# Optimization experiments

Hardware: AMD Instinct MI355X
Metric: run time of the kernel (lower is better)

## Reference

```python
import jax, jax.numpy as jnp
import numpy as np

# ---- config (YOLOv4-style, TRAIN_SIZE=608, P2..P5) ----
STRIDES = (4.0, 8.0, 16.0, 32.0)
ANCHORS = np.array([
    [[12, 16], [19, 36], [40, 28], [36, 75]],
    [[36, 75], [76, 55], [72, 146], [142, 110]],
    [[72, 146], [142, 110], [192, 243], [459, 401]],
    [[142, 110], [192, 243], [300, 300], [459, 401]],
], dtype=np.float32)  # [LEVELS, NUM_ANCHORS, 2]
MAX_PROP = 100
SCORE_THRESH = 0.25
IOU_THRESH = 0.5


def decode_prediction(p, anchors, stride):
    # p: [b, A, h, w, 6] -> [b, A*h*w, 5] with xyxy + score
    b, A, h, w, _ = p.shape
    txy, twh, conf, cls = p[..., :2], p[..., 2:4], p[..., 4:5], p[..., 5:6]
    gx, gy = jnp.meshgrid(jnp.arange(w, dtype=p.dtype), jnp.arange(h, dtype=p.dtype))
    grid = jnp.stack([gx, gy], axis=-1)[None, None]  # [1,1,h,w,2]
    xy = (jax.nn.sigmoid(txy) + grid) * stride
    wh = jnp.exp(twh) * anchors[None, :, None, None, :]
    score = jax.nn.sigmoid(conf) * jax.nn.sigmoid(cls)
    x1y1 = xy - 0.5 * wh
    x2y2 = xy + 0.5 * wh
    out = jnp.concatenate([x1y1, x2y2, score], axis=-1)  # [b,A,h,w,5]
    return out.reshape(b, A * h * w, 5)


def _iou_one_vs_all(box, boxes):
    # box: [4], boxes: [N,4] (xyxy)
    lt = jnp.maximum(box[:2], boxes[:, :2])
    rb = jnp.minimum(box[2:], boxes[:, 2:])
    wh = jnp.maximum(rb - lt, 0.0)
    inter = wh[:, 0] * wh[:, 1]
    a1 = jnp.maximum(box[2] - box[0], 0.0) * jnp.maximum(box[3] - box[1], 0.0)
    a2 = jnp.maximum(boxes[:, 2] - boxes[:, 0], 0.0) * jnp.maximum(boxes[:, 3] - boxes[:, 1], 0.0)
    return inter / (a1 + a2 - inter + 1e-9)


def _nms_single(boxes, scores):
    # greedy NMS, padded to MAX_PROP with zero rows
    s0 = jnp.where(scores >= SCORE_THRESH, scores, 0.0)

    def step(s, _):
        i = jnp.argmax(s)
        sc = s[i]
        box = boxes[i]
        keep = sc > 0.0
        row = jnp.where(keep, jnp.concatenate([box, sc[None]]), jnp.zeros(5, boxes.dtype))
        iou = _iou_one_vs_all(box, boxes)
        s = jnp.where((iou > IOU_THRESH) & keep, 0.0, s)
        s = s.at[i].set(0.0)
        return s, row

    _, props = jax.lax.scan(step, s0, None, length=MAX_PROP)
    return props  # [MAX_PROP, 5]


def entry_stop_gradients(t, mask):
    # gradient flows only through entries where mask==1
    return jax.lax.stop_gradient(t) * (1.0 - mask) + t * mask


def _forward(p2, p3, p4, p5):
    anchors = jnp.asarray(ANCHORS)
    d2 = decode_prediction(p2, anchors[0], STRIDES[0])
    d3 = decode_prediction(p3, anchors[1], STRIDES[1])
    d4 = decode_prediction(p4, anchors[2], STRIDES[2])
    d5 = decode_prediction(p5, anchors[3], STRIDES[3])
    proposals = jnp.concatenate([d2, d3, d4, d5], axis=1)  # [b, N, 5]
    proposals = jax.vmap(lambda pr: _nms_single(pr[:, :4], pr[:, 4]))(proposals)  # [b, MAX_PROP, 5]
    mask = (jnp.sum(proposals[..., :4], axis=-1) != 0.0).astype(proposals.dtype)[..., None]
    return entry_stop_gradients(proposals, mask)


def setup_inputs() -> dict:
    key = jax.random.key(0)
    k2, k3, k4, k5 = jax.random.split(key, 4)
    b, A, ch = 32, 4, 6
    return {
        "p2": jax.random.normal(k2, (b, A, 152, 152, ch), dtype=jnp.float32),
        "p3": jax.random.normal(k3, (b, A, 76, 76, ch), dtype=jnp.float32),
        "p4": jax.random.normal(k4, (b, A, 38, 38, ch), dtype=jnp.float32),
        "p5": jax.random.normal(k5, (b, A, 19, 19, ch), dtype=jnp.float32),
    }


def reference(p2, p3, p4, p5):
    return _forward(p2, p3, p4, p5)
```

## Files before the change

### kernel.cpp

```cpp
#include <hip/hip_runtime.h>
#include <cstdint>
#include <cstddef>

typedef unsigned int u32;
typedef unsigned long long u64;

#define NTOT 122740
#define NQ   30685
#define NPAIR 61370
#define KTOP 1024
#define WIN  256
#define NBIN 4096
#define SCORE_T 0.25f
#define TBITS 0x3E800000u
#define CSTRIDE 64


#define WS_COUNTERS 524288
#define WS_COMPACT  532480
#define WS_SCORES   794624

__device__ __forceinline__ float sigm(float x) { return 1.0f / (1.0f + expf(-x)); }

__device__ __forceinline__ int score_bin(u32 bits) {
  return min(4095, 1 + (int)((bits - TBITS) >> 12));
}

__device__ float4 decode_box_from_gidx(u32 gidx, int b,
    const float* __restrict__ p2, const float* __restrict__ p3,
    const float* __restrict__ p4, const float* __restrict__ p5)
{
  const float* p; int t, H, W; float stride;
  float aw0, ah0, aw1, ah1, aw2, ah2, aw3, ah3;
  if (gidx < 92416u) {
    p = p2 + (size_t)b * 92416 * 6; t = (int)gidx; H = 152; W = 152; stride = 4.0f;
    aw0=12.f; ah0=16.f; aw1=19.f; ah1=36.f; aw2=40.f; ah2=28.f; aw3=36.f; ah3=75.f;
  } else if (gidx < 115520u) {
    p = p3 + (size_t)b * 23104 * 6; t = (int)(gidx - 92416u); H = 76; W = 76; stride = 8.0f;
    aw0=36.f; ah0=75.f; aw1=76.f; ah1=55.f; aw2=72.f; ah2=146.f; aw3=142.f; ah3=110.f;
  } else if (gidx < 121296u) {
    p = p4 + (size_t)b * 5776 * 6; t = (int)(gidx - 115520u); H = 38; W = 38; stride = 16.0f;
    aw0=72.f; ah0=146.f; aw1=142.f; ah1=110.f; aw2=192.f; ah2=243.f; aw3=459.f; ah3=401.f;
  } else {
    p = p5 + (size_t)b * 1444 * 6; t = (int)(gidx - 121296u); H = 19; W = 19; stride = 32.0f;
    aw0=142.f; ah0=110.f; aw1=192.f; ah1=243.f; aw2=300.f; ah2=300.f; aw3=459.f; ah3=401.f;
  }
  int HW = H * W;
  int a = t / HW;
  int r = t - a * HW;
  int y = r / W;
  int x = r - y * W;
  const float* q = p + (size_t)t * 6;
  float2 t01 = *(const float2*)(q + 0);
  float2 t23 = *(const float2*)(q + 2);
  float cx = (sigm(t01.x) + (float)x) * stride;
  float cy = (sigm(t01.y) + (float)y) * stride;
  float aw = (a == 0) ? aw0 : (a == 1) ? aw1 : (a == 2) ? aw2 : aw3;
  float ah = (a == 0) ? ah0 : (a == 1) ? ah1 : (a == 2) ? ah2 : ah3;
  float bw = expf(t23.x) * aw;
  float bh = expf(t23.y) * ah;
  return make_float4(cx - 0.5f * bw, cy - 0.5f * bh, cx + 0.5f * bw, cy + 0.5f * bh);
}

__device__ __forceinline__ bool iou_gt(float4 A, float4 B) {
  float ltx = fmaxf(A.x, B.x), lty = fmaxf(A.y, B.y);
  float rbx = fminf(A.z, B.z), rby = fminf(A.w, B.w);
  float w = fmaxf(rbx - ltx, 0.0f), h = fmaxf(rby - lty, 0.0f);
  float inter = w * h;
  float a1 = fmaxf(A.z - A.x, 0.0f) * fmaxf(A.w - A.y, 0.0f);
  float a2 = fmaxf(B.z - B.x, 0.0f) * fmaxf(B.w - B.y, 0.0f);
  float iou = inter / (a1 + a2 - inter + 1e-9f);
  return iou > 0.5f;
}

__global__ __launch_bounds__(1024)
void zero_kernel(u32* w) {
  int t = blockIdx.x * 1024 + threadIdx.x;
  if (t < 133120) w[t] = 0u;
}

__global__ __launch_bounds__(256)
void decode_score_hist(const float* __restrict__ p2, const float* __restrict__ p3,
                       const float* __restrict__ p4, const float* __restrict__ p5,
                       u32* __restrict__ scores, u32* __restrict__ hist)
{
  __shared__ u32 lhist[NBIN];
  const int tid = threadIdx.x;
  const int b = blockIdx.y;
  for (int i = tid; i < NBIN; i += 256) lhist[i] = 0u;
  __syncthreads();

  uint2* srow = (uint2*)(scores + (size_t)b * NTOT);
  const int pbase = blockIdx.x * 2048;
  #pragma unroll 2
  for (int k = 0; k < 8; ++k) {
    int P = pbase + k * 256 + tid;
    if (P < NPAIR) {
      int t0 = 2 * P;
      const float* p; int l0, LN;
      if (t0 < 92416)       { p = p2; l0 = t0;          LN = 92416; }
      else if (t0 < 115520) { p = p3; l0 = t0 - 92416;  LN = 23104; }
      else if (t0 < 121296) { p = p4; l0 = t0 - 115520; LN = 5776;  }
      else                  { p = p5; l0 = t0 - 121296; LN = 1444;  }
      const float* q = p + ((size_t)b * LN + (size_t)l0) * 6 + 4;
      float4 v1 = *(const float4*)(q);
      float4 v2 = *(const float4*)(q + 4);
      float s0 = sigm(v1.x) * sigm(v1.y);
      float s1 = sigm(v2.z) * sigm(v2.w);
      u32 b0 = (s0 >= SCORE_T) ? __float_as_uint(s0) : 0u;
      u32 b1 = (s1 >= SCORE_T) ? __float_as_uint(s1) : 0u;
      srow[P] = make_uint2(b0, b1);
      if (b0) atomicAdd(&lhist[score_bin(b0)], 1u);
      if (b1) atomicAdd(&lhist[score_bin(b1)], 1u);
    }
  }
  __syncthreads();
  u32* gh = hist + (size_t)b * NBIN;
  for (int i = tid; i < NBIN; i += 256) {
    u32 v = lhist[i];
    if (v) atomicAdd(&gh[i], v);
  }
}

__global__ __launch_bounds__(256)
void filter_kernel(const u32* __restrict__ scores, const u32* __restrict__ hist,
                   u32* __restrict__ counters, uint2* __restrict__ compact)
{
  __shared__ u32 shist[NBIN];
  __shared__ u32 scan[256];
  __shared__ uint2 cand[KTOP];
  __shared__ u32 s_cnt, s_base;
  __shared__ int s_B;
  const int tid = threadIdx.x;
  const int b = blockIdx.y;

  const u32* gh = hist + (size_t)b * NBIN;
  for (int i = tid; i < NBIN; i += 256) shist[i] = gh[i];
  if (tid == 0) s_cnt = 0u;
  __syncthreads();

  u32 g = 0;
  const int base = tid * 16;
  #pragma unroll
  for (int k = 0; k < 16; ++k) g += shist[base + k];
  scan[tid] = g;
  __syncthreads();
  for (int off = 1; off < 256; off <<= 1) {
    u32 v = (tid + off < 256) ? scan[tid + off] : 0u;
    __syncthreads();
    scan[tid] += v;
    __syncthreads();
  }
  if (tid == 0 && scan[0] <= (u32)KTOP) s_B = 1;
  {
    u32 nxt = (tid < 255) ? scan[tid + 1] : 0u;
    if (scan[tid] > (u32)KTOP && nxt <= (u32)KTOP) {
      u32 c = nxt;
      int Bv = base + 16;
      for (int bin = base + 15; bin >= base; --bin) {
        c += shist[bin];
        if (c <= (u32)KTOP) Bv = bin; else break;
      }
      s_B = Bv;
    }
  }
  __syncthreads();
  const int B = max(s_B, 1);

  const uint4* sp = (const uint4*)(scores + (size_t)b * NTOT);
  const int i0 = blockIdx.x * 2048;
  const int i1 = min(i0 + 2048, NQ);
  for (int i = i0 + tid; i < i1; i += 256) {
    uint4 v = sp[i];
    u32 c4[4] = { v.x, v.y, v.z, v.w };
    #pragma unroll
    for (int c = 0; c < 4; ++c) {
      u32 bits = c4[c];
      if (bits && score_bin(bits) >= B) {
        u32 pos = atomicAdd(&s_cnt, 1u);
        if (pos < (u32)KTOP) cand[pos] = make_uint2(bits, (u32)(4 * i + c));
      }
    }
  }
  __syncthreads();
  const u32 m = min(s_cnt, (u32)KTOP);
  if (tid == 0) s_base = m ? atomicAdd(&counters[(size_t)b * CSTRIDE], m) : 0u;
  __syncthreads();
  const u32 gbase = s_base;
  uint2* crow = compact + (size_t)b * KTOP;
  for (u32 i = tid; i < m; i += 256) {
    u32 dst = gbase + i;
    if (dst < (u32)KTOP) crow[dst] = cand[i];
  }
}

__global__ __launch_bounds__(1024, 1)
void sort_nms_kernel(const uint2* __restrict__ compact, const u32* __restrict__ counters,
                     const float* __restrict__ p2, const float* __restrict__ p3,
                     const float* __restrict__ p4, const float* __restrict__ p5,
                     float* __restrict__ out)
{
  const int b = blockIdx.x;
  const int tid = threadIdx.x;

  __shared__ u64 skey[KTOP];
  __shared__ float4 sbox[WIN];
  __shared__ u64 smat[WIN * 4];
  __shared__ float4 selbox[100];
  __shared__ int s_misc[4];

  const int n = min((int)counters[(size_t)b * CSTRIDE], KTOP);
  const uint2* crow = compact + (size_t)b * KTOP;
  if (tid < n) {
    uint2 pr = crow[tid];
    skey[tid] = ~(((u64)pr.x << 32) | (u32)(~pr.y));
  } else {
    skey[tid] = ~0ull;
  }
  __syncthreads();

  for (int kk = 2; kk <= KTOP; kk <<= 1) {
    for (int jj = kk >> 1; jj > 0; jj >>= 1) {
      int i = tid, ixj = i ^ jj;
      if (ixj > i) {
        u64 a = skey[i], c = skey[ixj];
        bool up = ((i & kk) == 0);
        if ((a > c) == up) { skey[i] = c; skey[ixj] = a; }
      }
      __syncthreads();
    }
  }

  const int Wn = min(n, WIN);

  if (tid < WIN) {
    sbox[tid] = (tid < Wn) ? decode_box_from_gidx(~(u32)(~skey[tid]), b, p2, p3, p4, p5)
                           : make_float4(0.f, 0.f, 0.f, 0.f);
  }
  __syncthreads();

  {
    int row = tid >> 2, word = tid & 3;
    u64 bits = 0;
    if (row < Wn) {
      float4 A = sbox[row];
      int j0 = word * 64;
      int je = min(64, Wn - j0);
      for (int j = 0; j < je; ++j)
        if (iou_gt(A, sbox[j0 + j])) bits |= (1ull << j);
    }
    smat[tid] = bits;
  }
  __syncthreads();

  if (tid == 0) {
    u64 s0 = 0, s1 = 0, s2 = 0, s3 = 0;
    int sel = 0;
    for (int p = 0; p < Wn && sel < 100; ++p) {
      u64 sw = (p < 64) ? s0 : (p < 128) ? s1 : (p < 192) ? s2 : s3;
      if ((sw >> (p & 63)) & 1ull) continue;
      float4 box = sbox[p];
      u64 kcomp = ~skey[p];
      float sc = __uint_as_float((u32)(kcomp >> 32));
      selbox[sel] = box;
      float* orow = out + (size_t)b * 500 + (size_t)sel * 5;
      orow[0] = box.x; orow[1] = box.y; orow[2] = box.z; orow[3] = box.w; orow[4] = sc;
      sel++;
      s0 |= smat[p * 4 + 0]; s1 |= smat[p * 4 + 1];
      s2 |= smat[p * 4 + 2]; s3 |= smat[p * 4 + 3];
    }
    s_misc[2] = sel;
    s_misc[3] = (sel < 100 && n > WIN) ? 1 : 0;
  }
  __syncthreads();

  if (s_misc[3]) {
    if (tid < 64) {
      const int lane = tid;
      int sel = s_misc[2];
      for (int p = WIN; p < n && sel < 100; ++p) {
        u64 kcomp = ~skey[p];
        float4 box = decode_box_from_gidx(~(u32)kcomp, b, p2, p3, p4, p5);
        bool hit = false;
        if (lane < sel) hit = iou_gt(selbox[lane], box);
        if (lane + 64 < sel) hit = hit || iou_gt(selbox[lane + 64], box);
        u64 anyhit = __ballot(hit);
        if (anyhit == 0ull) {
          if (lane == 0) {
            selbox[sel] = box;
            float sc = __uint_as_float((u32)(kcomp >> 32));
            float* orow = out + (size_t)b * 500 + (size_t)sel * 5;
            orow[0] = box.x; orow[1] = box.y; orow[2] = box.z; orow[3] = box.w; orow[4] = sc;
          }
          sel++;
        }
      }
      if (lane == 0) s_misc[2] = sel;
    }
  }
  __syncthreads();

  const int nsel = s_misc[2];
  for (int i = tid; i < (100 - nsel) * 5; i += 1024)
    out[(size_t)b * 500 + (size_t)nsel * 5 + i] = 0.0f;
}

extern "C" void kernel_launch(void* const* d_in, const int* in_sizes, int n_in,
                              void* d_out, int out_size, void* d_ws, size_t ws_size,
                              hipStream_t stream) {
  const float* p2 = (const float*)d_in[0];
  const float* p3 = (const float*)d_in[1];
  const float* p4 = (const float*)d_in[2];
  const float* p5 = (const float*)d_in[3];
  float* out = (float*)d_out;

  unsigned char* w = (unsigned char*)d_ws;
  u32*   hist     = (u32*)w;
  u32*   counters = (u32*)(w + WS_COUNTERS);
  uint2* compact  = (uint2*)(w + WS_COMPACT);
  u32*   scores   = (u32*)(w + WS_SCORES);

  zero_kernel<<<130, 1024, 0, stream>>>(hist);
  decode_score_hist<<<dim3(30, 32), 256, 0, stream>>>(p2, p3, p4, p5, scores, hist);
  filter_kernel<<<dim3(15, 32), 256, 0, stream>>>(scores, hist, counters, compact);
  sort_nms_kernel<<<32, 1024, 0, stream>>>(compact, counters, p2, p3, p4, p5, out);
}
```

Baseline: 180.6 us.

## Fuse top-K filter into sort/NMS kernel and parallelize sort and NMS selection

The separate filter kernel and global compaction buffer are removed. Threshold selection and candidate compaction now run inside the per-image sort/NMS block, using wave-ballot aggregated atomics and a coarser 512-bin histogram. The bitonic sort uses register shuffles for strides under 64 and shared memory only for larger strides. The single-thread greedy NMS scan becomes a 64-lane ballot-driven loop whose results are written out in parallel. The zero kernel becomes a memset. The risk is that the filtering pass now runs on only 32 blocks, one per image, which limits parallelism for that phase.

```diff
diff --git a/kernel.cpp b/kernel.cpp
--- a/kernel.cpp
+++ b/kernel.cpp
@@ -10,20 +10,16 @@
 #define NPAIR 61370
 #define KTOP 1024
 #define WIN  256
-#define NBIN 4096
+#define NBIN 512
 #define SCORE_T 0.25f
 #define TBITS 0x3E800000u
-#define CSTRIDE 64
-
-
-#define WS_COUNTERS 524288
-#define WS_COMPACT  532480
-#define WS_SCORES   794624
+#define WS_SCORES 65536
+
 
 __device__ __forceinline__ float sigm(float x) { return 1.0f / (1.0f + expf(-x)); }
 
 __device__ __forceinline__ int score_bin(u32 bits) {
-  return min(4095, 1 + (int)((bits - TBITS) >> 12));
+  return min(NBIN - 1, 1 + (int)((bits - TBITS) >> 15));
 }
 
 __device__ float4 decode_box_from_gidx(u32 gidx, int b,
@@ -73,10 +69,22 @@
   return iou > 0.5f;
 }
 
-__global__ __launch_bounds__(1024)
-void zero_kernel(u32* w) {
-  int t = blockIdx.x * 1024 + threadIdx.x;
-  if (t < 133120) w[t] = 0u;
+__device__ __forceinline__ u64 shflx_u64(u64 v, int m) {
+  u32 lo = (u32)v, hi = (u32)(v >> 32);
+  lo = (u32)__shfl_xor((int)lo, m, 64);
+  hi = (u32)__shfl_xor((int)hi, m, 64);
+  return ((u64)hi << 32) | lo;
+}
+__device__ __forceinline__ u64 ce_pick(u64 v, u64 p, int i, int jj, int kk) {
+  bool up = ((i & kk) == 0);
+  bool low = ((i & jj) == 0);
+  u64 mn = (v < p) ? v : p;
+  u64 mx = (v < p) ? p : v;
+  return (low == up) ? mn : mx;
+}
+__device__ __forceinline__ u64 ce_shfl(u64 v, int i, int jj, int kk) {
+  u64 p = shflx_u64(v, jj);
+  return ce_pick(v, p, i, jj, kk);
 }
 
 __global__ __launch_bounds__(256)
@@ -92,7 +100,7 @@
 
   uint2* srow = (uint2*)(scores + (size_t)b * NTOT);
   const int pbase = blockIdx.x * 2048;
-  #pragma unroll 2
+  #pragma unroll 4
   for (int k = 0; k < 8; ++k) {
     int P = pbase + k * 256 + tid;
     if (P < NPAIR) {
@@ -122,114 +130,89 @@
   }
 }
 
-__global__ __launch_bounds__(256)
-void filter_kernel(const u32* __restrict__ scores, const u32* __restrict__ hist,
-                   u32* __restrict__ counters, uint2* __restrict__ compact)
-{
-  __shared__ u32 shist[NBIN];
-  __shared__ u32 scan[256];
-  __shared__ uint2 cand[KTOP];
-  __shared__ u32 s_cnt, s_base;
-  __shared__ int s_B;
-  const int tid = threadIdx.x;
-  const int b = blockIdx.y;
-
-  const u32* gh = hist + (size_t)b * NBIN;
-  for (int i = tid; i < NBIN; i += 256) shist[i] = gh[i];
-  if (tid == 0) s_cnt = 0u;
-  __syncthreads();
-
-  u32 g = 0;
-  const int base = tid * 16;
-  #pragma unroll
-  for (int k = 0; k < 16; ++k) g += shist[base + k];
-  scan[tid] = g;
-  __syncthreads();
-  for (int off = 1; off < 256; off <<= 1) {
-    u32 v = (tid + off < 256) ? scan[tid + off] : 0u;
-    __syncthreads();
-    scan[tid] += v;
-    __syncthreads();
-  }
-  if (tid == 0 && scan[0] <= (u32)KTOP) s_B = 1;
-  {
-    u32 nxt = (tid < 255) ? scan[tid + 1] : 0u;
-    if (scan[tid] > (u32)KTOP && nxt <= (u32)KTOP) {
-      u32 c = nxt;
-      int Bv = base + 16;
-      for (int bin = base + 15; bin >= base; --bin) {
-        c += shist[bin];
-        if (c <= (u32)KTOP) Bv = bin; else break;
-      }
-      s_B = Bv;
-    }
-  }
-  __syncthreads();
-  const int B = max(s_B, 1);
-
-  const uint4* sp = (const uint4*)(scores + (size_t)b * NTOT);
-  const int i0 = blockIdx.x * 2048;
-  const int i1 = min(i0 + 2048, NQ);
-  for (int i = i0 + tid; i < i1; i += 256) {
-    uint4 v = sp[i];
-    u32 c4[4] = { v.x, v.y, v.z, v.w };
-    #pragma unroll
-    for (int c = 0; c < 4; ++c) {
-      u32 bits = c4[c];
-      if (bits && score_bin(bits) >= B) {
-        u32 pos = atomicAdd(&s_cnt, 1u);
-        if (pos < (u32)KTOP) cand[pos] = make_uint2(bits, (u32)(4 * i + c));
-      }
-    }
-  }
-  __syncthreads();
-  const u32 m = min(s_cnt, (u32)KTOP);
-  if (tid == 0) s_base = m ? atomicAdd(&counters[(size_t)b * CSTRIDE], m) : 0u;
-  __syncthreads();
-  const u32 gbase = s_base;
-  uint2* crow = compact + (size_t)b * KTOP;
-  for (u32 i = tid; i < m; i += 256) {
-    u32 dst = gbase + i;
-    if (dst < (u32)KTOP) crow[dst] = cand[i];
-  }
-}
-
 __global__ __launch_bounds__(1024, 1)
-void sort_nms_kernel(const uint2* __restrict__ compact, const u32* __restrict__ counters,
+void sort_nms_kernel(const u32* __restrict__ scores, const u32* __restrict__ hist,
                      const float* __restrict__ p2, const float* __restrict__ p3,
                      const float* __restrict__ p4, const float* __restrict__ p5,
                      float* __restrict__ out)
 {
   const int b = blockIdx.x;
   const int tid = threadIdx.x;
-
+  const int lane = tid & 63;
+
+  __shared__ u32 shist[NBIN];
+  __shared__ u32 sc[NBIN];
+  __shared__ uint2 cand[KTOP];
   __shared__ u64 skey[KTOP];
   __shared__ float4 sbox[WIN];
   __shared__ u64 smat[WIN * 4];
   __shared__ float4 selbox[100];
-  __shared__ int s_misc[4];
-
-  const int n = min((int)counters[(size_t)b * CSTRIDE], KTOP);
-  const uint2* crow = compact + (size_t)b * KTOP;
-  if (tid < n) {
-    uint2 pr = crow[tid];
-    skey[tid] = ~(((u64)pr.x << 32) | (u32)(~pr.y));
-  } else {
-    skey[tid] = ~0ull;
-  }
-  __syncthreads();
-
-  for (int kk = 2; kk <= KTOP; kk <<= 1) {
-    for (int jj = kk >> 1; jj > 0; jj >>= 1) {
-      int i = tid, ixj = i ^ jj;
-      if (ixj > i) {
-        u64 a = skey[i], c = skey[ixj];
-        bool up = ((i & kk) == 0);
-        if ((a > c) == up) { skey[i] = c; skey[ixj] = a; }
+  __shared__ u32 sellist[100];
+  __shared__ u32 s_cnt;
+  __shared__ int s_B, s_nsel, s_slow;
+
+  const u32* gh = hist + (size_t)b * NBIN;
+  if (tid < NBIN) { u32 h = gh[tid]; shist[tid] = h; sc[tid] = h; }
+  if (tid == 0) { s_cnt = 0u; s_B = NBIN - 1; s_slow = 0; }
+  __syncthreads();
+  for (int off = 1; off < NBIN; off <<= 1) {
+    u32 v = 0;
+    if (tid < NBIN && tid + off < NBIN) v = sc[tid + off];
+    __syncthreads();
+    if (tid < NBIN) sc[tid] += v;
+    __syncthreads();
+  }
+  if (tid < NBIN) {
+    if (sc[tid] <= (u32)KTOP && (tid == 0 || sc[tid - 1] > (u32)KTOP))
+      s_B = max((int)tid, 1);
+  }
+  __syncthreads();
+  const int B = s_B;
+
+  const uint4* sp = (const uint4*)(scores + (size_t)b * NTOT);
+  for (int i = tid; i < NQ; i += 1024) {
+    uint4 v = sp[i];
+    u32 c4[4] = { v.x, v.y, v.z, v.w };
+    #pragma unroll
+    for (int c = 0; c < 4; ++c) {
+      u32 bits = c4[c];
+      bool pred = bits && (score_bin(bits) >= B);
+      u64 m = __ballot(pred);
+      if (m) {
+        int leader = (int)__ffsll((unsigned long long)m) - 1;
+        u32 base = 0;
+        if (lane == leader) base = atomicAdd(&s_cnt, (u32)__popcll(m));
+        base = (u32)__shfl((int)base, leader, 64);
+        if (pred) {
+          u32 pos = base + (u32)__popcll(m & ((1ull << lane) - 1ull));
+          if (pos < (u32)KTOP) cand[pos] = make_uint2(bits, (u32)(4 * i + c));
+        }
       }
-      __syncthreads();
-    }
-  }
+    }
+  }
+  __syncthreads();
+  const int n = min((int)s_cnt, KTOP);
+
+  u64 v;
+  if (tid < n) { uint2 pr = cand[tid]; v = ~(((u64)pr.x << 32) | (u32)(~pr.y)); }
+  else v = ~0ull;
+  const int i = tid;
+  #pragma unroll
+  for (int kk = 2; kk <= 64; kk <<= 1)
+    #pragma unroll
+    for (int jj = kk >> 1; jj > 0; jj >>= 1)
+      v = ce_shfl(v, i, jj, kk);
+  for (int kk = 128; kk <= KTOP; kk <<= 1) {
+    for (int jj = kk >> 1; jj >= 64; jj >>= 1) {
+      skey[i] = v; __syncthreads();
+      u64 p = skey[i ^ jj]; __syncthreads();
+      v = ce_pick(v, p, i, jj, kk);
+    }
+    #pragma unroll
+    for (int jj = 32; jj > 0; jj >>= 1) v = ce_shfl(v, i, jj, kk);
+  }
+  skey[i] = v;
+  __syncthreads();
 
   const int Wn = min(n, WIN);
 
@@ -244,8 +227,7 @@
     u64 bits = 0;
     if (row < Wn) {
       float4 A = sbox[row];
-      int j0 = word * 64;
-      int je = min(64, Wn - j0);
+      int j0 = word * 64, je = min(64, Wn - j0);
       for (int j = 0; j < je; ++j)
         if (iou_gt(A, sbox[j0 + j])) bits |= (1ull << j);
     }
@@ -253,31 +235,56 @@
   }
   __syncthreads();
 
-  if (tid == 0) {
-    u64 s0 = 0, s1 = 0, s2 = 0, s3 = 0;
+  if (tid < 64) {
+    u64 m0[4], m1[4], m2[4], m3[4];
+    #pragma unroll
+    for (int d = 0; d < 4; ++d) {
+      m0[d] = smat[(lane      ) * 4 + d];
+      m1[d] = smat[(lane +  64) * 4 + d];
+      m2[d] = smat[(lane + 128) * 4 + d];
+      m3[d] = smat[(lane + 192) * 4 + d];
+    }
+    bool f0 = lane < Wn, f1 = lane + 64 < Wn, f2 = lane + 128 < Wn, f3 = lane + 192 < Wn;
     int sel = 0;
-    for (int p = 0; p < Wn && sel < 100; ++p) {
-      u64 sw = (p < 64) ? s0 : (p < 128) ? s1 : (p < 192) ? s2 : s3;
-      if ((sw >> (p & 63)) & 1ull) continue;
-      float4 box = sbox[p];
-      u64 kcomp = ~skey[p];
-      float sc = __uint_as_float((u32)(kcomp >> 32));
-      selbox[sel] = box;
-      float* orow = out + (size_t)b * 500 + (size_t)sel * 5;
-      orow[0] = box.x; orow[1] = box.y; orow[2] = box.z; orow[3] = box.w; orow[4] = sc;
+    while (sel < 100) {
+      u64 b0 = __ballot(f0), b1 = __ballot(f1), b2 = __ballot(f2), b3 = __ballot(f3);
+      int p;
+      if (b0)      p = (int)__ffsll((unsigned long long)b0) - 1;
+      else if (b1) p = 64 + (int)__ffsll((unsigned long long)b1) - 1;
+      else if (b2) p = 128 + (int)__ffsll((unsigned long long)b2) - 1;
+      else if (b3) p = 192 + (int)__ffsll((unsigned long long)b3) - 1;
+      else break;
+      if (lane == 0) sellist[sel] = (u32)p;
       sel++;
-      s0 |= smat[p * 4 + 0]; s1 |= smat[p * 4 + 1];
-      s2 |= smat[p * 4 + 2]; s3 |= smat[p * 4 + 3];
-    }
-    s_misc[2] = sel;
-    s_misc[3] = (sel < 100 && n > WIN) ? 1 : 0;
-  }
-  __syncthreads();
-
-  if (s_misc[3]) {
+      int d = p >> 6, sh = p & 63;
+      u64 r0 = (d == 0) ? m0[0] : (d == 1) ? m0[1] : (d == 2) ? m0[2] : m0[3];
+      u64 r1 = (d == 0) ? m1[0] : (d == 1) ? m1[1] : (d == 2) ? m1[2] : m1[3];
+      u64 r2 = (d == 0) ? m2[0] : (d == 1) ? m2[1] : (d == 2) ? m2[2] : m2[3];
+      u64 r3 = (d == 0) ? m3[0] : (d == 1) ? m3[1] : (d == 2) ? m3[2] : m3[3];
+      f0 = f0 && !((r0 >> sh) & 1);
+      f1 = f1 && !((r1 >> sh) & 1);
+      f2 = f2 && !((r2 >> sh) & 1);
+      f3 = f3 && !((r3 >> sh) & 1);
+    }
+    if (lane == 0) { s_nsel = sel; s_slow = (sel < 100 && n > WIN) ? 1 : 0; }
+  }
+  __syncthreads();
+
+  const int nsel0 = s_nsel;
+  if (tid < nsel0) {
+    u32 p = sellist[tid];
+    float4 bx = sbox[p];
+    u64 kcomp = ~skey[p];
+    float scs = __uint_as_float((u32)(kcomp >> 32));
+    float* orow = out + (size_t)b * 500 + (size_t)tid * 5;
+    orow[0] = bx.x; orow[1] = bx.y; orow[2] = bx.z; orow[3] = bx.w; orow[4] = scs;
+  }
+
+  if (s_slow) {
+    if (tid < nsel0) selbox[tid] = sbox[sellist[tid]];
+    __syncthreads();
     if (tid < 64) {
-      const int lane = tid;
-      int sel = s_misc[2];
+      int sel = nsel0;
       for (int p = WIN; p < n && sel < 100; ++p) {
         u64 kcomp = ~skey[p];
         float4 box = decode_box_from_gidx(~(u32)kcomp, b, p2, p3, p4, p5);
@@ -288,21 +295,21 @@
         if (anyhit == 0ull) {
           if (lane == 0) {
             selbox[sel] = box;
-            float sc = __uint_as_float((u32)(kcomp >> 32));
+            float scs = __uint_as_float((u32)(kcomp >> 32));
             float* orow = out + (size_t)b * 500 + (size_t)sel * 5;
-            orow[0] = box.x; orow[1] = box.y; orow[2] = box.z; orow[3] = box.w; orow[4] = sc;
+            orow[0] = box.x; orow[1] = box.y; orow[2] = box.z; orow[3] = box.w; orow[4] = scs;
           }
           sel++;
         }
       }
-      if (lane == 0) s_misc[2] = sel;
-    }
-  }
-  __syncthreads();
-
-  const int nsel = s_misc[2];
-  for (int i = tid; i < (100 - nsel) * 5; i += 1024)
-    out[(size_t)b * 500 + (size_t)nsel * 5 + i] = 0.0f;
+      if (lane == 0) s_nsel = sel;
+    }
+  }
+  __syncthreads();
+
+  const int nsel = s_nsel;
+  for (int k = tid; k < (100 - nsel) * 5; k += 1024)
+    out[(size_t)b * 500 + (size_t)nsel * 5 + k] = 0.0f;
 }
 
 extern "C" void kernel_launch(void* const* d_in, const int* in_sizes, int n_in,
@@ -314,14 +321,10 @@
   const float* p5 = (const float*)d_in[3];
   float* out = (float*)d_out;
 
-  unsigned char* w = (unsigned char*)d_ws;
-  u32*   hist     = (u32*)w;
-  u32*   counters = (u32*)(w + WS_COUNTERS);
-  uint2* compact  = (uint2*)(w + WS_COMPACT);
-  u32*   scores   = (u32*)(w + WS_SCORES);
-
-  zero_kernel<<<130, 1024, 0, stream>>>(hist);
+  u32* hist   = (u32*)d_ws;
+  u32* scores = (u32*)((unsigned char*)d_ws + WS_SCORES);
+
+  hipMemsetAsync(hist, 0, WS_SCORES, stream);
   decode_score_hist<<<dim3(30, 32), 256, 0, stream>>>(p2, p3, p4, p5, scores, hist);
-  filter_kernel<<<dim3(15, 32), 256, 0, stream>>>(scores, hist, counters, compact);
-  sort_nms_kernel<<<32, 1024, 0, stream>>>(compact, counters, p2, p3, p4, p5, out);
-}
+  sort_nms_kernel<<<32, 1024, 0, stream>>>(scores, hist, p2, p3, p4, p5, out);
+}
```

After: 196.8 us. 9.0% more time.
